# Optimization experiments

Hardware: AMD Instinct MI355X
Metric: run time of the kernel (lower is better)

Reference implementation:

```python
import jax, jax.numpy as jnp
import numpy as np

B, C, L = 8, 256, 2048      # batch, res_channels, seq_len
E = 2 * C                    # attention / S4 width = 512
CH = 4                       # S4 channels
SQRT_HALF = 0.7071067811865476


def setup_inputs() -> dict:
    key = jax.random.key(0)
    ks = jax.random.split(key, 12)
    def n(k, s, sc):
        return jax.random.normal(k, s, dtype=jnp.float32) * sc
    return dict(
        x=jax.random.normal(ks[0], (B, C, L), dtype=jnp.float32),
        original=jax.random.normal(ks[1], (B, C, L), dtype=jnp.float32),
        sn_scale=jnp.ones((1, C, 1), jnp.float32),
        conv_w=n(ks[2], (E, C, 3), 0.05), conv_b=jnp.zeros((E,), jnp.float32),
        s4_ln_g=jnp.ones((E,), jnp.float32), s4_ln_b=jnp.zeros((E,), jnp.float32),
        s4_kernel=n(ks[3], (CH, E, L), 0.01),           # long-conv kernel per channel
        s4_D=n(ks[4], (CH, E), 1.0),                     # skip connection D
        s4_out_w=n(ks[5], (E, CH * E), 0.02), s4_out_b=jnp.zeros((E,), jnp.float32),
        attn_v_w=n(ks[6], (E, E), 0.02), attn_v_b=jnp.zeros((E,), jnp.float32),
        attn_o_w=n(ks[7], (E, E), 0.02), attn_o_b=jnp.zeros((E,), jnp.float32),
        res_w=n(ks[8], (C, C, 1), 0.05), res_b=jnp.zeros((C,), jnp.float32),
        skip_w=n(ks[9], (C, C, 1), 0.05), skip_b=jnp.zeros((C,), jnp.float32),
    )


def reference(x, original, sn_scale, conv_w, conv_b, s4_ln_g, s4_ln_b,
              s4_kernel, s4_D, s4_out_w, s4_out_b,
              attn_v_w, attn_v_b, attn_o_w, attn_o_b,
              res_w, res_b, skip_w, skip_b):
    eps = 1e-8
    # RMSNorm over channel dim (dim=1)
    rms = jnp.sqrt(jnp.sum(x * x, axis=1, keepdims=True)) / np.sqrt(x.shape[1]).astype(np.float32)
    x_n = sn_scale * x / (rms + eps)
    # h = x + original (pre-norm x), conv k=3 pad=1, GELU
    h = x + original
    h = jax.lax.conv_general_dilated(h, conv_w, (1,), [(1, 1)],
                                     dimension_numbers=('NCH', 'OIH', 'NCH'))
    h = jax.nn.gelu(h + conv_b[None, :, None], approximate=False)
    # --- S4 / GConv: LN over channels, FFT causal long conv, D-skip, GELU, out linear ---
    mu = h.mean(axis=1, keepdims=True)
    var = h.var(axis=1, keepdims=True)
    u = (h - mu) / jnp.sqrt(var + 1e-5) * s4_ln_g[None, :, None] + s4_ln_b[None, :, None]
    n2 = 2 * u.shape[-1]
    uf = jnp.fft.rfft(u, n=n2)                      # (B, E, F)
    kf = jnp.fft.rfft(s4_kernel, n=n2)              # (CH, E, F)
    y = jnp.fft.irfft(jnp.einsum('bhf,chf->bchf', uf, kf), n=n2)[..., :u.shape[-1]]
    y = y + s4_D[None, :, :, None] * u[:, None]     # (B, CH, E, L)
    y = jax.nn.gelu(y.reshape(y.shape[0], CH * E, y.shape[-1]), approximate=False)
    h_t = jnp.einsum('oc,bcl->bol', s4_out_w, y) + s4_out_b[None, :, None]  # (B, E, L)
    # --- local-window MHA with window_size=1: each position attends only to itself,
    # softmax over a single unmasked score == 1, so out = Wo @ (Wv @ x + bv) + bo exactly ---
    v = jnp.einsum('oe,bel->bol', attn_v_w, h_t) + attn_v_b[None, :, None]
    h_s = jnp.einsum('oe,bel->bol', attn_o_w, v) + attn_o_b[None, :, None]
    h2 = h_t + h_s
    out = jnp.tanh(h2[:, :C]) * jax.nn.sigmoid(h2[:, C:])
    res = jnp.einsum('oc,bcl->bol', res_w[:, :, 0], out) + res_b[None, :, None]
    skip = jnp.einsum('oc,bcl->bol', skip_w[:, :, 0], out) + skip_b[None, :, None]
    return ((x_n + res) * SQRT_HALF, skip)
```

## Files before the change

kernel.cpp:

```cpp
#include <hip/hip_runtime.h>
#include <hip/hip_bf16.h>
#include <math.h>

typedef __attribute__((ext_vector_type(8))) short short8;
typedef __attribute__((ext_vector_type(4))) float float4_t;
typedef __attribute__((ext_vector_type(2))) float cf2;
typedef unsigned short ushort_t;
typedef unsigned int uint_t;

#define NBL 16384

#define WS_CONVA   ((size_t)0)
#define WS_WV      ((size_t)786432)
#define WS_WO      ((size_t)1310720)
#define WS_W1      ((size_t)1835008)
#define WS_WCAT    ((size_t)3932160)
#define WS_A2      ((size_t)4194304)
#define WS_ACOMB   ((size_t)4718592)
#define WS_BCOMB   ((size_t)6815744)
#define WS_XN      ((size_t)6819840)
#define WS_H0PT    ((size_t)23597056)
#define WS_U       ((size_t)31993856)
#define WS_GT      ((size_t)65548288)
#define WS_UF      WS_GT
#define WS_KF      ((size_t)99102720)
#define WS_G       ((size_t)132657152)
#define WS_GATET   (WS_G + 25165824)
#define WS_UB      ((size_t)208162816)

__device__ __forceinline__ float gelu_f(float x) {
    float t = x * x;
    float a2 = x * fmaf(0.07135481627f, t, 1.59576912161f);
    return x / (1.f + __expf(-a2));
}
__device__ __forceinline__ float tanh_f(float a) {
    return 1.f - 2.f / (1.f + __expf(2.f * a));
}
__device__ __forceinline__ float sigmoid_f(float b) {
    return 1.f / (1.f + __expf(-b));
}

__device__ __forceinline__ unsigned int pack_bf2(float a, float b) {
#if __has_builtin(__builtin_amdgcn_cvt_pk_bf16_f32)
    auto v = __builtin_amdgcn_cvt_pk_bf16_f32(a, b);
    unsigned int r; __builtin_memcpy(&r, &v, 4); return r;
#else
    __hip_bfloat16 ha = __float2bfloat16(a), hb = __float2bfloat16(b);
    unsigned short ua = *(unsigned short*)&ha, ub = *(unsigned short*)&hb;
    return (unsigned int)ua | ((unsigned int)ub << 16);
#endif
}
__device__ __forceinline__ ushort_t f2bfu(float a) {
    __hip_bfloat16 h = __float2bfloat16(a);
    return *(ushort_t*)&h;
}
__device__ __forceinline__ cf2 unpack_c(unsigned int v) {
    cf2 r;
    r.x = __uint_as_float(v << 16);
    r.y = __uint_as_float(v & 0xffff0000u);
    return r;
}
__device__ __forceinline__ float bf2f(ushort_t u) {
    return __uint_as_float(((unsigned int)u) << 16);
}

__device__ __forceinline__ void cp16(const ushort_t* g, ushort_t* l) {
    __builtin_amdgcn_global_load_lds(
        (__attribute__((address_space(1))) void*)(void*)g,
        (__attribute__((address_space(3))) void*)l, 16, 0, 0);
}

__device__ __forceinline__ cf2 cswap(cf2 a) { return __builtin_shufflevector(a, a, 1, 0); }
template<int SGN>
__device__ __forceinline__ cf2 cmuli(cf2 a) {
    cf2 s = cswap(a);
    return s * cf2{(float)(-SGN), (float)SGN};
}
__device__ __forceinline__ cf2 cmul(cf2 a, cf2 b) {
    cf2 t = cswap(a) * cf2{-b.y, b.y};
    return a * cf2{b.x, b.x} + t;
}
__device__ __forceinline__ cf2 cmulc(cf2 a, float wr, float wi) {
    cf2 t = cswap(a) * cf2{-wi, wi};
    return a * cf2{wr, wr} + t;
}

__global__ __launch_bounds__(256) void wprep_kernel(
    const float* __restrict__ conv_w, const float* __restrict__ attn_v_w,
    const float* __restrict__ attn_o_w, const float* __restrict__ s4_out_w,
    const float* __restrict__ res_w, const float* __restrict__ skip_w,
    __hip_bfloat16* __restrict__ convA, __hip_bfloat16* __restrict__ WvT,
    __hip_bfloat16* __restrict__ WoBf, __hip_bfloat16* __restrict__ W1T,
    __hip_bfloat16* __restrict__ Wcat)
{
    const int N0 = 393216, N1 = 655360, N2c = 917504, N3 = 1966080, N4 = 2097152;
    for (int i = blockIdx.x * 256 + threadIdx.x; i < N4; i += gridDim.x * 256) {
        if (i < N0) {
            int m = i / 768, r = i - m * 768, dk = r >> 8, c = r & 255;
            convA[i] = __float2bfloat16(conv_w[m * 768 + c * 3 + dk]);
        } else if (i < N1) {
            int j = i - N0; int row = j >> 9, e = j & 511;
            WvT[j] = __float2bfloat16(attn_v_w[e * 512 + row]);
        } else if (i < N2c) {
            WoBf[i - N1] = __float2bfloat16(attn_o_w[i - N1]);
        } else if (i < N3) {
            int j = i - N2c; int ck = j >> 9, e = j & 511;
            W1T[j] = __float2bfloat16(s4_out_w[e * 2048 + ck]);
        } else {
            int j = i - N3; int m = j >> 8, c = j & 255;
            float v = (m < 256) ? res_w[m * 256 + c] : skip_w[(m - 256) * 256 + c];
            Wcat[j] = __float2bfloat16(v);
        }
    }
}

__global__ __launch_bounds__(256) void bias2_kernel(
    const __hip_bfloat16* __restrict__ A2, const float* __restrict__ s4_out_b,
    const float* __restrict__ attn_o_w, const float* __restrict__ attn_v_b,
    const float* __restrict__ attn_o_b, float* __restrict__ bcomb)
{
    __shared__ float red[256];
    int o = blockIdx.x, t = threadIdx.x;
    float s = 0.f;
    for (int e = t; e < 512; e += 256)
        s += __bfloat162float(A2[o * 512 + e]) * s4_out_b[e] + attn_o_w[o * 512 + e] * attn_v_b[e];
    red[t] = s; __syncthreads();
    for (int k = 128; k > 0; k >>= 1) { if (t < k) red[t] += red[t + k]; __syncthreads(); }
    if (t == 0) bcomb[o] = red[0] + attn_o_b[o];
}

__global__ __launch_bounds__(512) void prep_kernel(
    const float* __restrict__ x, const float* __restrict__ orig,
    const float* __restrict__ sn, ushort_t* __restrict__ xnb, ushort_t* __restrict__ h0pT)
{
    __shared__ float red[8][64];
    __shared__ ushort_t T[256 * 66];
    int blk = blockIdx.x, t = threadIdx.x;
    int lane = t & 63, cg = t >> 6;
    int b = blk >> 5, l0 = (blk & 31) << 6;
    size_t basein = (size_t)b * 524288 + l0 + lane;
    float ss = 0.f;
    for (int c = cg; c < 256; c += 8) {
        size_t idx = basein + (size_t)c * 2048;
        float xv = x[idx], ov = orig[idx];
        ss += xv * xv;
        T[c * 66 + lane] = f2bfu(xv + ov);
    }
    red[cg][lane] = ss;
    __syncthreads();
    float tot = 0.f;
    #pragma unroll
    for (int k = 0; k < 8; ++k) tot += red[k][lane];
    float inv = 1.0f / (sqrtf(tot) * 0.0625f + 1e-8f);
    __hip_bfloat16* xo = (__hip_bfloat16*)xnb;
    for (int c = cg; c < 256; c += 8) {
        size_t idx = basein + (size_t)c * 2048;
        xo[idx] = __float2bfloat16(sn[c] * x[idx] * inv);
    }
    int c2 = t & 255, half = t >> 8;
    size_t rowbase = (size_t)(b * 2050 + 1 + l0);
    for (int r = half; r < 64; r += 2)
        h0pT[(rowbase + r) * 256 + c2] = T[c2 * 66 + r];
    if ((blk & 31) == 0) {
        if (t < 256) h0pT[(size_t)(b * 2050) * 256 + t] = 0;
        else         h0pT[(size_t)(b * 2050 + 2049) * 256 + (t - 256)] = 0;
    }
}

__global__ __launch_bounds__(512) void ln_kernel(
    const ushort_t* __restrict__ h, ushort_t* __restrict__ ub,
    const float* __restrict__ gam, const float* __restrict__ bet)
{
    __shared__ float r1[8][64], r2[8][64];
    int blk = blockIdx.x, t = threadIdx.x;
    int lane = t & 63, og = t >> 6;
    int n = (blk << 6) + lane;
    float s1 = 0.f, s2 = 0.f;
    for (int o = og; o < 512; o += 8) { float v = bf2f(h[(size_t)o * NBL + n]); s1 += v; s2 += v * v; }
    r1[og][lane] = s1; r2[og][lane] = s2;
    __syncthreads();
    float mu = 0.f, m2 = 0.f;
    #pragma unroll
    for (int k = 0; k < 8; ++k) { mu += r1[k][lane]; m2 += r2[k][lane]; }
    mu *= (1.f / 512.f); m2 *= (1.f / 512.f);
    float rstd = rsqrtf(m2 - mu * mu + 1e-5f);
    int b = n >> 11, l = n & 2047;
    size_t sbase = (size_t)(b >> 1) * 4096 + 2 * l + (b & 1);
    for (int o = og; o < 512; o += 8) {
        size_t idx = (size_t)o * NBL + n;
        ub[(size_t)o * 16384 + sbase] = f2bfu((bf2f(h[idx]) - mu) * rstd * gam[o] + bet[o]);
    }
}

#define PERM(m) ((((m) & 3) << 2) | ((m) >> 2))

template<int SGN>
__device__ __forceinline__ void dft4p(cf2& a0, cf2& a1, cf2& a2, cf2& a3) {
    cf2 t0 = a0 + a2, t1 = a0 - a2, t2 = a1 + a3, t3 = a1 - a3;
    cf2 j3 = cmuli<SGN>(t3);
    a0 = t0 + t2; a2 = t0 - t2;
    a1 = t1 + j3; a3 = t1 - j3;
}
template<int SGN>
__device__ __forceinline__ void dft4p_half(cf2& a0, cf2& a1, cf2& a2, cf2& a3) {
    cf2 u0 = a0, u1 = a1;
    cf2 j1 = cmuli<SGN>(u1);
    a0 = u0 + u1; a2 = u0 - u1;
    a1 = u0 + j1; a3 = u0 - j1;
}
template<int SGN>
__device__ __forceinline__ void dft4p_out01(cf2 a0, cf2 a1, cf2 a2, cf2 a3, cf2& o0, cf2& o1) {
    cf2 t0 = a0 + a2, t1 = a0 - a2, t2 = a1 + a3, t3 = a1 - a3;
    o0 = t0 + t2;
    o1 = t1 + cmuli<SGN>(t3);
}

template<int SGN>
__device__ __forceinline__ void dft16_stepB(cf2* x) {
    const float sg = (float)SGN;
    const float C16[10] = {1.f, 0.92387953f, 0.70710678f, 0.38268343f, 0.f,
                           -0.38268343f, -0.70710678f, -0.92387953f, -1.f, -0.92387953f};
    const float S16[10] = {0.f, 0.38268343f, 0.70710678f, 0.92387953f, 1.f,
                           0.92387953f, 0.70710678f, 0.38268343f, 0.f, -0.38268343f};
    #pragma unroll
    for (int s = 1; s < 4; ++s)
        #pragma unroll
        for (int r = 1; r < 4; ++r) {
            int e = s * r;
            x[4 * s + r] = cmulc(x[4 * s + r], C16[e], sg * S16[e]);
        }
}
template<int SGN>
__device__ __forceinline__ void dft16p(cf2* x) {
    #pragma unroll
    for (int r = 0; r < 4; ++r) dft4p<SGN>(x[r], x[4 + r], x[8 + r], x[12 + r]);
    dft16_stepB<SGN>(x);
    #pragma unroll
    for (int s = 0; s < 4; ++s) dft4p<SGN>(x[4 * s], x[4 * s + 1], x[4 * s + 2], x[4 * s + 3]);
}
template<int SGN>
__device__ __forceinline__ void dft16_halfin(cf2* x) {
    #pragma unroll
    for (int r = 0; r < 4; ++r) dft4p_half<SGN>(x[r], x[4 + r], x[8 + r], x[12 + r]);
    dft16_stepB<SGN>(x);
    #pragma unroll
    for (int s = 0; s < 4; ++s) dft4p<SGN>(x[4 * s], x[4 * s + 1], x[4 * s + 2], x[4 * s + 3]);
}
template<int SGN>
__device__ __forceinline__ void dft16_halfout(cf2* x, cf2* y) {
    #pragma unroll
    for (int r = 0; r < 4; ++r) dft4p<SGN>(x[r], x[4 + r], x[8 + r], x[12 + r]);
    dft16_stepB<SGN>(x);
    #pragma unroll
    for (int s = 0; s < 4; ++s)
        dft4p_out01<SGN>(x[4 * s], x[4 * s + 1], x[4 * s + 2], x[4 * s + 3], y[s], y[4 + s]);
}

template<int SGN>
__device__ __forceinline__ void tw_after(cf2* x, float p, float invQ) {
    float s1, c1; __sincosf((float)SGN * 6.283185307179586f * p * invQ, &s1, &c1);
    cf2 w1 = {c1, s1}, w = w1;
    #pragma unroll
    for (int m = 1; m < 16; ++m) { x[PERM(m)] = cmul(x[PERM(m)], w); w = cmul(w, w1); }
}
template<int SGN>
__device__ __forceinline__ void tw_before(cf2* x, float p, float invQ) {
    float s1, c1; __sincosf((float)SGN * 6.283185307179586f * p * invQ, &s1, &c1);
    cf2 w1 = {c1, s1}, w = w1;
    #pragma unroll
    for (int j = 1; j < 16; ++j) { x[j] = cmul(x[j], w); w = cmul(w, w1); }
}

__global__ __launch_bounds__(256) void fft_fwd_kernel(
    const ushort_t* __restrict__ ubf, const float* __restrict__ s4k,
    uint4* __restrict__ uf, uint4* __restrict__ kf)
{
    __shared__ cf2 S[4368];
    int wg = blockIdx.x, t = threadIdx.x;
    cf2 x[16];
    if (wg < 2048) {
        int bp = wg >> 9, e = wg & 511;
        const unsigned int* p0 = (const unsigned int*)ubf + (size_t)e * 8192 + (size_t)bp * 2048;
        #pragma unroll
        for (int j = 0; j < 8; ++j) x[j] = unpack_c(p0[j * 256 + t]);
    } else {
        const float* p0 = s4k + (size_t)(wg - 2048) * 2048;
        #pragma unroll
        for (int j = 0; j < 8; ++j) x[j] = cf2{p0[j * 256 + t], 0.f};
    }
    dft16_halfin<-1>(x);
    tw_after<-1>(x, (float)t, 1.f / 4096.f);
    int tb = 17 * (t >> 4) + (t & 15);
    #pragma unroll
    for (int m = 0; m < 16; ++m) S[tb + 273 * m] = x[PERM(m)];
    __syncthreads();
    int b2 = 273 * (t >> 4) + (t & 15);
    #pragma unroll
    for (int j = 0; j < 16; ++j) x[j] = S[b2 + 17 * j];
    dft16p<-1>(x);
    tw_after<-1>(x, (float)(t & 15), 1.f / 256.f);
    #pragma unroll
    for (int m = 0; m < 16; ++m) S[b2 + 17 * m] = x[PERM(m)];
    __syncthreads();
    int b3 = 273 * (t >> 4) + 17 * (t & 15);
    #pragma unroll
    for (int j = 0; j < 16; ++j) x[j] = S[b3 + j];
    dft16p<-1>(x);
    const float sc = (wg < 2048) ? 1.f : (1.f / 4096.f);
    uint4* dst = ((wg < 2048) ? (uf + (size_t)wg * 1024) : (kf + (size_t)(wg - 2048) * 1024)) + 4 * t;
    #pragma unroll
    for (int q = 0; q < 4; ++q) {
        uint4 o;
        cf2 v0 = x[PERM(4 * q)] * sc, v1 = x[PERM(4 * q + 1)] * sc;
        cf2 v2 = x[PERM(4 * q + 2)] * sc, v3 = x[PERM(4 * q + 3)] * sc;
        o.x = pack_bf2(v0.x, v0.y);
        o.y = pack_bf2(v1.x, v1.y);
        o.z = pack_bf2(v2.x, v2.y);
        o.w = pack_bf2(v3.x, v3.y);
        dst[q] = o;
    }
}

__global__ __launch_bounds__(256) void fft_inv_kernel(
    const uint4* __restrict__ uf, const uint4* __restrict__ kf,
    unsigned int* __restrict__ g2)
{
    __shared__ cf2 S[4368];
    int wg = blockIdx.x, t = threadIdx.x;
    int bp = wg >> 11, ch = (wg >> 9) & 3, e = wg & 511;
    const uint4* zr = uf + (size_t)(bp * 512 + e) * 1024 + 4 * t;
    const uint4* kr = kf + (size_t)(ch * 512 + e) * 1024 + 4 * t;
    cf2 x[16];
    #pragma unroll
    for (int q = 0; q < 4; ++q) {
        uint4 a4 = zr[q], b4 = kr[q];
        x[4 * q + 0] = cmul(unpack_c(a4.x), unpack_c(b4.x));
        x[4 * q + 1] = cmul(unpack_c(a4.y), unpack_c(b4.y));
        x[4 * q + 2] = cmul(unpack_c(a4.z), unpack_c(b4.z));
        x[4 * q + 3] = cmul(unpack_c(a4.w), unpack_c(b4.w));
    }
    dft16p<1>(x);
    int b1 = 273 * (t >> 4) + 17 * (t & 15);
    #pragma unroll
    for (int m = 0; m < 16; ++m) S[b1 + m] = x[PERM(m)];
    __syncthreads();
    int b2 = 273 * (t >> 4) + (t & 15);
    #pragma unroll
    for (int j = 0; j < 16; ++j) x[j] = S[b2 + 17 * j];
    tw_before<1>(x, (float)(t & 15), 1.f / 256.f);
    dft16p<1>(x);
    #pragma unroll
    for (int m = 0; m < 16; ++m) S[b2 + 17 * m] = x[PERM(m)];
    __syncthreads();
    int b3 = 17 * (t >> 4) + (t & 15);
    #pragma unroll
    for (int j = 0; j < 16; ++j) x[j] = S[b3 + 273 * j];
    tw_before<1>(x, (float)t, 1.f / 4096.f);
    cf2 y[8];
    dft16_halfout<1>(x, y);
    unsigned int* go = g2 + (size_t)(ch * 512 + e) * 8192 + (size_t)bp * 2048;
    #pragma unroll
    for (int m = 0; m < 8; ++m)
        go[m * 256 + t] = pack_bf2(y[m].x, y[m].y);
}

__global__ __launch_bounds__(256) void gdt_kernel(
    const unsigned int* __restrict__ g2, const unsigned int* __restrict__ ub2,
    const float* __restrict__ s4D, ushort_t* __restrict__ gT)
{
    __shared__ unsigned int S2[64 * 65];
    int c0 = blockIdx.x * 64, r0 = blockIdx.y * 64;
    int t = threadIdx.x, lx = t & 63, ly0 = t >> 6;
    #pragma unroll
    for (int ly = ly0; ly < 64; ly += 4) {
        int r = r0 + ly, cp = c0 + lx;
        cf2 y2 = unpack_c(g2[(size_t)r * 8192 + cp]);
        cf2 u2 = unpack_c(ub2[(size_t)(r & 511) * 8192 + cp]);
        float d = s4D[r];
        float v0 = gelu_f(fmaf(d, u2.x, y2.x));
        float v1 = gelu_f(fmaf(d, u2.y, y2.y));
        S2[ly * 65 + lx] = pack_bf2(v0, v1);
    }
    __syncthreads();
    int rr = r0 + lx;
    size_t rpart = (size_t)(rr >> 5) * 524288 + (size_t)(((rr >> 3) & 3) * 128 + (rr & 7));
    #pragma unroll
    for (int ly = ly0; ly < 64; ly += 4) {
        int oc = c0 + ly;
        unsigned int v = S2[lx * 65 + ly];
        int bp = oc >> 11, l = oc & 2047;
        int n_lo = bp * 4096 + l;
        size_t npart = (size_t)(n_lo >> 6) * 2048 + (size_t)(((n_lo >> 4) & 3) * 512 + (n_lo & 15) * 8);
        gT[rpart + npart]         = (ushort_t)(v & 0xffff);
        gT[rpart + npart + 65536] = (ushort_t)(v >> 16);
    }
}

__global__ __launch_bounds__(256) void gemmF_kernel(
    const ushort_t* __restrict__ Af, const ushort_t* __restrict__ Bf,
    ushort_t* __restrict__ Cb, const float* __restrict__ bias)
{
    __shared__ ushort_t SM[8704];
    const int t = threadIdx.x;
    const int w = t >> 6, lane = t & 63, quad = lane >> 4, lr = lane & 15;
    const int wm = (w >> 1) * 64;
    const int by = blockIdx.y, n0 = blockIdx.x * 128;
    const int h = (w >> 1) ? (4 + by) : by;
    const int nb = (n0 >> 6) + (w & 1);

    const ushort_t* Aw = Af + (size_t)h * 2048 + (size_t)lane * 8;
    const ushort_t* Bw = Bf + (size_t)nb * 2048 + (size_t)lane * 8;

    float4_t acc[4][4];
    #pragma unroll
    for (int i = 0; i < 4; ++i)
        #pragma unroll
        for (int j = 0; j < 4; ++j) { float4_t z = {0.f, 0.f, 0.f, 0.f}; acc[i][j] = z; }

    short8 a0[4], a1[4], b0[4], b1[4];

#define LDA(D, S) do { _Pragma("unroll") for (int i_ = 0; i_ < 4; ++i_) \
        D[i_] = *(const short8*)(Aw + (size_t)(S) * 16384 + i_ * 512); } while (0)
#define LDB(D, S) do { _Pragma("unroll") for (int i_ = 0; i_ < 4; ++i_) \
        D[i_] = *(const short8*)(Bw + (size_t)(S) * 524288 + i_ * 512); } while (0)
#define CMP(AA, BB) do { _Pragma("unroll") for (int im_ = 0; im_ < 4; ++im_) \
        _Pragma("unroll") for (int in_ = 0; in_ < 4; ++in_) \
            acc[im_][in_] = __builtin_amdgcn_mfma_f32_16x16x32_bf16(AA[im_], BB[in_], acc[im_][in_], 0, 0, 0); } while (0)

    LDA(a0, 0); LDB(b0, 0);
    LDA(a1, 1); LDB(b1, 1);
    for (int s = 0; s < 64; s += 2) {
        CMP(a0, b0);
        if (s + 2 < 64) { LDA(a0, s + 2); LDB(b0, s + 2); }
        CMP(a1, b1);
        if (s + 3 < 64) { LDA(a1, s + 3); LDB(b1, s + 3); }
    }
#undef LDA
#undef LDB
#undef CMP

    #pragma unroll
    for (int p = 0; p < 2; ++p) {
        if (p) __syncthreads();
        if ((w & 1) == p) {
            #pragma unroll
            for (int im = 0; im < 4; ++im)
                #pragma unroll
                for (int in_ = 0; in_ < 4; ++in_) {
                    int nl = in_ * 16 + lr;
                    #pragma unroll
                    for (int r = 0; r < 4; ++r) {
                        int i = wm + im * 16 + quad * 4 + r;
                        int me = (i < 64) ? (64 * by + i) : (192 + 64 * by + i);
                        SM[i * 68 + nl] = f2bfu(acc[im][in_][r] + bias[me]);
                    }
                }
        }
        __syncthreads();
        int nl = t >> 2, gcb = (t & 3) * 16;
        size_t obase = (size_t)(n0 + 64 * p + nl) * 256 + 64 * by + gcb;
        short8 o0, o1;
        #pragma unroll
        for (int j = 0; j < 16; ++j) {
            int gc = gcb + j;
            float a = bf2f(SM[gc * 68 + nl]);
            float bb = bf2f(SM[(gc + 64) * 68 + nl]);
            ushort_t gv = f2bfu(tanh_f(a) * sigmoid_f(bb));
            if (j < 8) o0[j] = (short)gv; else o1[j - 8] = (short)gv;
        }
        *(short8*)(Cb + obase) = o0;
        *(short8*)(Cb + obase + 8) = o1;
    }
}

template<int BSRC, int EPI>
__global__ __launch_bounds__(256, 4) void gemm_kernel(
    const ushort_t* __restrict__ A, const ushort_t* __restrict__ Bm,
    ushort_t* __restrict__ Cb, float* __restrict__ Cf,
    int M, int N, int K,
    const float* __restrict__ bias, const float* __restrict__ bias2,
    const ushort_t* __restrict__ xnb, float* __restrict__ dout)
{
    __shared__ ushort_t SM[16384];
    const int t = threadIdx.x;
    const int n0 = blockIdx.x * 64, m0 = blockIdx.y * 128;
    const int w = t >> 6, lane = t & 63, quad = lane >> 4, lr = lane & 15;
    const int wm = (w >> 1) * 64, wn = (w & 1) * 32;

    const int srow = lane >> 2;
    const int swslot = ((lane & 3) ^ ((lane >> 3) & 3)) * 8;
    const int r0q = w * 32 + srow;
    int ar0 = m0 + r0q, ar1 = m0 + r0q + 16;
    const ushort_t* aSrc0 = A + (size_t)ar0 * K + swslot;
    const ushort_t* aSrc1 = A + (size_t)ar1 * K + swslot;
    const int nrow = n0 + w * 16 + srow;
    const ushort_t* bSrc;
    if (BSRC == 0) bSrc = Bm + (size_t)nrow * K + swslot;
    else           bSrc = Bm + (size_t)((nrow >> 11) * 2050 + (nrow & 2047)) * 256 + swslot;

    const int aD = w * 1024;
    const int bD = 4096 + w * 512;

    float4_t acc[4][2];
    #pragma unroll
    for (int i = 0; i < 4; ++i)
        #pragma unroll
        for (int j = 0; j < 2; ++j) { float4_t z = {0.f, 0.f, 0.f, 0.f}; acc[i][j] = z; }

    const int qsw = (quad ^ ((lr >> 1) & 3)) << 3;

#define STAGE(BUF, KK) do {                                                     \
        cp16(aSrc0 + (KK), SM + (BUF) + aD);                                    \
        cp16(aSrc1 + (KK), SM + (BUF) + aD + 512);                              \
        if (BSRC == 0) cp16(bSrc + (KK), SM + (BUF) + bD);                      \
        else cp16(bSrc + (((KK) >> 8) * 256 + ((KK) & 255)), SM + (BUF) + bD);  \
    } while (0)

#define COMPUTE(BUF) do {                                                       \
        const ushort_t* Al = SM + (BUF);                                        \
        const ushort_t* Bl = SM + (BUF) + 4096;                                 \
        short8 af[4], bfr[2];                                                   \
        _Pragma("unroll")                                                       \
        for (int im = 0; im < 4; ++im)                                          \
            af[im] = *(const short8*)&Al[(wm + im * 16 + lr) * 32 + qsw];       \
        _Pragma("unroll")                                                       \
        for (int in_ = 0; in_ < 2; ++in_)                                       \
            bfr[in_] = *(const short8*)&Bl[(wn + in_ * 16 + lr) * 32 + qsw];    \
        _Pragma("unroll")                                                       \
        for (int im = 0; im < 4; ++im)                                          \
            _Pragma("unroll")                                                   \
            for (int in_ = 0; in_ < 2; ++in_)                                   \
                acc[im][in_] = __builtin_amdgcn_mfma_f32_16x16x32_bf16(         \
                    af[im], bfr[in_], acc[im][in_], 0, 0, 0);                   \
    } while (0)

    STAGE(0, 0);
    __syncthreads();

    for (int kt = 0; kt < K; kt += 64) {
        STAGE(8192, kt + 32);
        COMPUTE(0);
        __syncthreads();
        if (kt + 64 < K) STAGE(0, kt + 64);
        COMPUTE(8192);
        __syncthreads();
    }
#undef STAGE
#undef COMPUTE

    #pragma unroll
    for (int im = 0; im < 4; ++im) {
        #pragma unroll
        for (int in_ = 0; in_ < 2; ++in_) {
            int n = n0 + wn + in_ * 16 + lr;
            int mb = m0 + wm + im * 16 + quad * 4;
            #pragma unroll
            for (int r = 0; r < 4; ++r) {
                int m = mb + r;
                float v = acc[im][in_][r];
                if (EPI == 0) {
                    v += bias[m];
                    ((__hip_bfloat16*)Cb)[(size_t)m * N + n] = __float2bfloat16(gelu_f(v));
                } else if (EPI == 1) {
                    v += (m == n) ? 1.0f : 0.0f;
                    ((__hip_bfloat16*)Cb)[(size_t)m * N + n] = __float2bfloat16(v);
                } else if (EPI == 2) {
                    size_t fi = ((((size_t)(n >> 5) * 8 + (m >> 6)) * 4 + ((m >> 4) & 3)) * 64
                                 + ((n >> 3) & 3) * 16 + (m & 15)) * 8 + (n & 7);
                    Cb[fi] = f2bfu(v);
                } else {
                    int bb = n >> 11, ll = n & 2047;
                    if (m < 256) {
                        v += bias[m];
                        int idx = (bb << 19) + (m << 11) + ll;
                        dout[idx] = (bf2f(xnb[idx]) + v) * 0.70710678118654752f;
                    } else {
                        v += bias2[m - 256];
                        dout[4194304 + (bb << 19) + ((m - 256) << 11) + ll] = v;
                    }
                }
            }
        }
    }
}

extern "C" void kernel_launch(void* const* d_in, const int* in_sizes, int n_in,
                              void* d_out, int out_size, void* d_ws, size_t ws_size,
                              hipStream_t stream)
{
    const float* x         = (const float*)d_in[0];
    const float* original  = (const float*)d_in[1];
    const float* sn_scale  = (const float*)d_in[2];
    const float* conv_w    = (const float*)d_in[3];
    const float* conv_b    = (const float*)d_in[4];
    const float* s4_ln_g   = (const float*)d_in[5];
    const float* s4_ln_b   = (const float*)d_in[6];
    const float* s4_kernel = (const float*)d_in[7];
    const float* s4_D      = (const float*)d_in[8];
    const float* s4_out_w  = (const float*)d_in[9];
    const float* s4_out_b  = (const float*)d_in[10];
    const float* attn_v_w  = (const float*)d_in[11];
    const float* attn_v_b  = (const float*)d_in[12];
    const float* attn_o_w  = (const float*)d_in[13];
    const float* attn_o_b  = (const float*)d_in[14];
    const float* res_w     = (const float*)d_in[15];
    const float* res_b     = (const float*)d_in[16];
    const float* skip_w    = (const float*)d_in[17];
    const float* skip_b    = (const float*)d_in[18];

    char* ws = (char*)d_ws;
    __hip_bfloat16* convA = (__hip_bfloat16*)(ws + WS_CONVA);
    __hip_bfloat16* WvT   = (__hip_bfloat16*)(ws + WS_WV);
    __hip_bfloat16* WoBf  = (__hip_bfloat16*)(ws + WS_WO);
    __hip_bfloat16* W1T   = (__hip_bfloat16*)(ws + WS_W1);
    __hip_bfloat16* Wcat  = (__hip_bfloat16*)(ws + WS_WCAT);
    ushort_t* A2    = (ushort_t*)(ws + WS_A2);
    ushort_t* Acomb = (ushort_t*)(ws + WS_ACOMB);
    float* bcombp  = (float*)(ws + WS_BCOMB);
    ushort_t* xnb  = (ushort_t*)(ws + WS_XN);
    ushort_t* h0pT = (ushort_t*)(ws + WS_H0PT);
    ushort_t* hP   = (ushort_t*)(ws + WS_U);
    ushort_t* ubP  = (ushort_t*)(ws + WS_UB);
    uint4* ufP = (uint4*)(ws + WS_UF);
    uint4* kfP = (uint4*)(ws + WS_KF);
    unsigned int* g2P = (unsigned int*)(ws + WS_G);
    ushort_t* gT    = (ushort_t*)(ws + WS_GT);
    ushort_t* gateT = (ushort_t*)(ws + WS_GATET);

    wprep_kernel<<<dim3(4096), dim3(256), 0, stream>>>(conv_w, attn_v_w, attn_o_w, s4_out_w,
        res_w, skip_w, convA, WvT, WoBf, W1T, Wcat);
    gemm_kernel<0, 1><<<dim3(8, 4), dim3(256), 0, stream>>>(
        (const ushort_t*)WoBf, (const ushort_t*)WvT, A2, nullptr, 512, 512, 512,
        nullptr, nullptr, nullptr, nullptr);
    bias2_kernel<<<dim3(512), dim3(256), 0, stream>>>(
        (const __hip_bfloat16*)A2, s4_out_b, attn_o_w, attn_v_b, attn_o_b, bcombp);
    gemm_kernel<0, 2><<<dim3(32, 4), dim3(256), 0, stream>>>(
        A2, (const ushort_t*)W1T, Acomb, nullptr, 512, 2048, 512,
        nullptr, nullptr, nullptr, nullptr);

    prep_kernel<<<dim3(256), dim3(512), 0, stream>>>(x, original, sn_scale, xnb, h0pT);
    gemm_kernel<1, 0><<<dim3(256, 4), dim3(256), 0, stream>>>(
        (const ushort_t*)convA, h0pT, hP, nullptr, 512, NBL, 768,
        conv_b, nullptr, nullptr, nullptr);
    ln_kernel<<<dim3(256), dim3(512), 0, stream>>>(hP, ubP, s4_ln_g, s4_ln_b);
    fft_fwd_kernel<<<dim3(4096), dim3(256), 0, stream>>>(ubP, s4_kernel, ufP, kfP);
    fft_inv_kernel<<<dim3(8192), dim3(256), 0, stream>>>(ufP, kfP, g2P);
    gdt_kernel<<<dim3(128, 32), dim3(256), 0, stream>>>(
        g2P, (const unsigned int*)ubP, s4_D, gT);
    gemmF_kernel<<<dim3(128, 4), dim3(256), 0, stream>>>(
        (const ushort_t*)Acomb, gT, gateT, bcombp);
    gemm_kernel<0, 4><<<dim3(256, 4), dim3(256), 0, stream>>>(
        (const ushort_t*)Wcat, gateT, nullptr, nullptr, 512, NBL, 256,
        res_b, skip_b, xnb, (float*)d_out);
}
```

Baseline: 423.5 us.

## Fuse D-skip, GELU and transposed store into inverse FFT kernel

Removes the separate gdt kernel by applying the D-skip, GELU and scatter into the GEMM-friendly gT layout directly in the inverse FFT epilogue. This avoids writing and re-reading the intermediate g2 buffer. Block ordering is remapped so consecutive blocks cover neighbouring e/ch/bp and store into nearby gT regions. The scattered 2-byte stores now come straight from the FFT lanes without the shared-memory transpose, which may coalesce poorly.

```diff
diff --git a/kernel.cpp b/kernel.cpp
--- a/kernel.cpp
+++ b/kernel.cpp
@@ -21,11 +21,10 @@
 #define WS_XN      ((size_t)6819840)
 #define WS_H0PT    ((size_t)23597056)
 #define WS_U       ((size_t)31993856)
-#define WS_GT      ((size_t)65548288)
-#define WS_UF      WS_GT
+#define WS_UF      ((size_t)65548288)
 #define WS_KF      ((size_t)99102720)
-#define WS_G       ((size_t)132657152)
-#define WS_GATET   (WS_G + 25165824)
+#define WS_GTF     ((size_t)132657152)
+#define WS_GATET   ((size_t)199766016)
 #define WS_UB      ((size_t)208162816)
 
 __device__ __forceinline__ float gelu_f(float x) {
@@ -323,11 +322,14 @@
 
 __global__ __launch_bounds__(256) void fft_inv_kernel(
     const uint4* __restrict__ uf, const uint4* __restrict__ kf,
-    unsigned int* __restrict__ g2)
+    const unsigned int* __restrict__ ub2, const float* __restrict__ s4D,
+    ushort_t* __restrict__ gT)
 {
     __shared__ cf2 S[4368];
-    int wg = blockIdx.x, t = threadIdx.x;
-    int bp = wg >> 11, ch = (wg >> 9) & 3, e = wg & 511;
+    int bid = blockIdx.x, t = threadIdx.x;
+    int tau = (bid & 7) * 1024 + (bid >> 3);
+    int e = tau >> 4, ch = (tau >> 2) & 3, bp = tau & 3;
+    int r = ch * 512 + e;
     const uint4* zr = uf + (size_t)(bp * 512 + e) * 1024 + 4 * t;
     const uint4* kr = kf + (size_t)(ch * 512 + e) * 1024 + 4 * t;
     cf2 x[16];
@@ -358,41 +360,20 @@
     tw_before<1>(x, (float)t, 1.f / 4096.f);
     cf2 y[8];
     dft16_halfout<1>(x, y);
-    unsigned int* go = g2 + (size_t)(ch * 512 + e) * 8192 + (size_t)bp * 2048;
-    #pragma unroll
-    for (int m = 0; m < 8; ++m)
-        go[m * 256 + t] = pack_bf2(y[m].x, y[m].y);
-}
-
-__global__ __launch_bounds__(256) void gdt_kernel(
-    const unsigned int* __restrict__ g2, const unsigned int* __restrict__ ub2,
-    const float* __restrict__ s4D, ushort_t* __restrict__ gT)
-{
-    __shared__ unsigned int S2[64 * 65];
-    int c0 = blockIdx.x * 64, r0 = blockIdx.y * 64;
-    int t = threadIdx.x, lx = t & 63, ly0 = t >> 6;
-    #pragma unroll
-    for (int ly = ly0; ly < 64; ly += 4) {
-        int r = r0 + ly, cp = c0 + lx;
-        cf2 y2 = unpack_c(g2[(size_t)r * 8192 + cp]);
-        cf2 u2 = unpack_c(ub2[(size_t)(r & 511) * 8192 + cp]);
-        float d = s4D[r];
-        float v0 = gelu_f(fmaf(d, u2.x, y2.x));
-        float v1 = gelu_f(fmaf(d, u2.y, y2.y));
-        S2[ly * 65 + lx] = pack_bf2(v0, v1);
-    }
-    __syncthreads();
-    int rr = r0 + lx;
-    size_t rpart = (size_t)(rr >> 5) * 524288 + (size_t)(((rr >> 3) & 3) * 128 + (rr & 7));
-    #pragma unroll
-    for (int ly = ly0; ly < 64; ly += 4) {
-        int oc = c0 + ly;
-        unsigned int v = S2[lx * 65 + ly];
-        int bp = oc >> 11, l = oc & 2047;
+
+    const float d = s4D[r];
+    const unsigned int* ur = ub2 + (size_t)e * 8192 + (size_t)bp * 2048 + t;
+    const size_t rpart = (size_t)(r >> 5) * 524288 + (size_t)(((r >> 3) & 3) * 128 + (r & 7));
+    #pragma unroll
+    for (int m = 0; m < 8; ++m) {
+        int l = m * 256 + t;
+        cf2 u2 = unpack_c(ur[m * 256]);
+        float v0 = gelu_f(fmaf(d, u2.x, y[m].x));
+        float v1 = gelu_f(fmaf(d, u2.y, y[m].y));
         int n_lo = bp * 4096 + l;
         size_t npart = (size_t)(n_lo >> 6) * 2048 + (size_t)(((n_lo >> 4) & 3) * 512 + (n_lo & 15) * 8);
-        gT[rpart + npart]         = (ushort_t)(v & 0xffff);
-        gT[rpart + npart + 65536] = (ushort_t)(v >> 16);
+        gT[rpart + npart]         = f2bfu(v0);
+        gT[rpart + npart + 65536] = f2bfu(v1);
     }
 }
 
@@ -623,8 +604,7 @@
     ushort_t* ubP  = (ushort_t*)(ws + WS_UB);
     uint4* ufP = (uint4*)(ws + WS_UF);
     uint4* kfP = (uint4*)(ws + WS_KF);
-    unsigned int* g2P = (unsigned int*)(ws + WS_G);
-    ushort_t* gT    = (ushort_t*)(ws + WS_GT);
+    ushort_t* gT    = (ushort_t*)(ws + WS_GTF);
     ushort_t* gateT = (ushort_t*)(ws + WS_GATET);
 
     wprep_kernel<<<dim3(4096), dim3(256), 0, stream>>>(conv_w, attn_v_w, attn_o_w, s4_out_w,
@@ -644,9 +624,8 @@
         conv_b, nullptr, nullptr, nullptr);
     ln_kernel<<<dim3(256), dim3(512), 0, stream>>>(hP, ubP, s4_ln_g, s4_ln_b);
     fft_fwd_kernel<<<dim3(4096), dim3(256), 0, stream>>>(ubP, s4_kernel, ufP, kfP);
-    fft_inv_kernel<<<dim3(8192), dim3(256), 0, stream>>>(ufP, kfP, g2P);
-    gdt_kernel<<<dim3(128, 32), dim3(256), 0, stream>>>(
-        g2P, (const unsigned int*)ubP, s4_D, gT);
+    fft_inv_kernel<<<dim3(8192), dim3(256), 0, stream>>>(
+        ufP, kfP, (const unsigned int*)ubP, s4_D, gT);
     gemmF_kernel<<<dim3(128, 4), dim3(256), 0, stream>>>(
         (const ushort_t*)Acomb, gT, gateT, bcombp);
     gemm_kernel<0, 4><<<dim3(256, 4), dim3(256), 0, stream>>>(
```

Measured after the change: 388.0 us. 8.4% less time.
